# Kernel optimization log

Measured on AMD Instinct MI355X. Metric: run time of the kernel, lower is better.

The kernel has to match this reference:

```python
import jax, jax.numpy as jnp
import numpy as np

DILATIONS = (1, 2, 4, 8)
K = 3  # kernel_size
B, H, W, C = 16, 128, 128, 64
HID = 256
OUT = 64  # == C, so residual path is taken


def _depthwise(x, w, dilation):
    # x: [B,H,W,C], w: [K,K,1,C] (HWIO depthwise kernel)
    pad = dilation * (K // 2)
    return jax.lax.conv_general_dilated(
        x, w,
        window_strides=(1, 1),
        padding=[(pad, pad), (pad, pad)],
        rhs_dilation=(dilation, dilation),
        dimension_numbers=('NHWC', 'HWIO', 'NHWC'),
        feature_group_count=C,
    )


def setup_inputs() -> dict:
    key = jax.random.key(0)
    k_x, k_cw, k_w1, k_b1, k_w2, k_b2 = jax.random.split(key, 6)
    in_feat = C * (1 + len(DILATIONS))  # 320
    x = jax.random.normal(k_x, (B, H, W, C), jnp.float32)
    # depthwise kernels, one [K,K,1,C] per dilation, stacked
    conv_w = jax.random.normal(k_cw, (len(DILATIONS), K, K, 1, C), jnp.float32) * (1.0 / np.sqrt(K * K).astype(np.float32))
    W1 = jax.random.normal(k_w1, (in_feat, HID), jnp.float32) * np.float32(1.0 / np.sqrt(in_feat))
    b1 = jax.random.normal(k_b1, (HID,), jnp.float32) * 0.01
    W2 = jax.random.normal(k_w2, (HID, OUT), jnp.float32) * np.float32(1.0 / np.sqrt(HID))
    b2 = jax.random.normal(k_b2, (OUT,), jnp.float32) * 0.01
    return {"x": x, "conv_w": conv_w, "W1": W1, "b1": b1, "W2": W2, "b2": b2}


def reference(x, conv_w, W1, b1, W2, b2):
    # 1) Perception: multiscale depthwise dilated convs (same-padding per dilation)
    perceptions = [_depthwise(x, conv_w[i], d) for i, d in enumerate(DILATIONS)]
    upd_in = jnp.concatenate([x] + perceptions, axis=-1)  # [B,H,W,5C]
    # 2) Update MLP: Linear -> Dropout(eval: identity) -> GELU(exact erf) -> Linear
    h = jax.nn.gelu(upd_in @ W1 + b1, approximate=False)  # [B,H,W,HID]
    delta = h @ W2 + b2  # [B,H,W,OUT]
    # 3) out_channels == channels and (eval mode or fire_rate==1.0): plain residual
    return x + delta
```

## Files before the change

### kernel.cpp

```cpp
#include <hip/hip_runtime.h>
#include <cstdint>

#define B_   16
#define H_   128
#define W_   128
#define C_   64
#define HID_ 256
#define XELEMS (B_ * H_ * W_ * C_)

typedef _Float16 __attribute__((ext_vector_type(2))) half2v;
typedef _Float16 __attribute__((ext_vector_type(8))) half8v;
typedef __attribute__((ext_vector_type(4))) float f32x4;
typedef unsigned short ushort_t;

#define W1S_OFF 0
#define W2S_OFF 81920
#define CWH_OFF 98304
#define XH_OFF  100608
#define WS_NEED_BYTES (2u * XH_OFF + 2u * XELEMS)

__device__ __forceinline__ int hs(int row, int col) {
  return row * 256 + (((col >> 3) ^ (row & 7)) << 3) + (col & 7);
}

__device__ __forceinline__ float fast_gelu(float h) {
  float u = h * fmaf(h * h, 0.10293921f, 2.30211813f);
  float e = exp2f(-u);
  return h * __builtin_amdgcn_rcpf(1.0f + e);
}

__global__ void cvt_x_kernel(const float* __restrict__ x,
                             _Float16* __restrict__ xh) {
  int i = (blockIdx.x * 256 + threadIdx.x) * 8;
  const float4 a = *(const float4*)&x[i];
  const float4 b = *(const float4*)&x[i + 4];
  half8v o = {(_Float16)a.x, (_Float16)a.y, (_Float16)a.z, (_Float16)a.w,
              (_Float16)b.x, (_Float16)b.y, (_Float16)b.z, (_Float16)b.w};
  *(half8v*)&xh[i] = o;
}

__global__ void cvt_weights_kernel(const float* __restrict__ W1,
                                   const float* __restrict__ W2,
                                   const float* __restrict__ cw,
                                   _Float16* __restrict__ w1s,
                                   _Float16* __restrict__ w2s,
                                   _Float16* __restrict__ cwh) {
  int t = blockIdx.x * 256 + threadIdx.x;
  if (t < 81920) {
    int j = t & 7, lane = (t >> 3) & 63, n16 = (t >> 9) & 15, ks = t >> 13;
    int k = ks * 32 + (lane >> 4) * 8 + j;
    int n = n16 * 16 + (lane & 15);
    w1s[t] = (_Float16)W1[k * 256 + n];
  } else if (t < 98304) {
    int t2 = t - 81920;
    int j = t2 & 7, lane = (t2 >> 3) & 63, n16 = (t2 >> 9) & 3, ks = t2 >> 11;
    int k = ks * 32 + (lane >> 4) * 8 + j;
    int n = n16 * 16 + (lane & 15);
    w2s[t2] = (_Float16)W2[k * 64 + n];
  } else if (t < 98304 + 2304) {
    int t3 = t - 98304;
    cwh[t3] = (_Float16)cw[t3];
  }
}

template <bool BOUND, bool FP16X>
__device__ __forceinline__ void conv_phase(const float* __restrict__ xb,
                                           const _Float16* __restrict__ xhb,
                                           const _Float16* __restrict__ cwh,
                                           ushort_t* __restrict__ feat,
                                           int tid, int tileX, int tileY) {
  const int quad = tid & 15;
  const int p0   = tid >> 4;
#pragma unroll
  for (int dd = 0; dd < 4; ++dd) {
    const int dil = 1 << dd;
    half2v w01[9], w23[9];
#pragma unroll
    for (int t = 0; t < 9; ++t) {
      uint2 wr = *(const uint2*)&cwh[(dd * 9 + t) * C_ + quad * 4];
      w01[t] = __builtin_bit_cast(half2v, wr.x);
      w23[t] = __builtin_bit_cast(half2v, wr.y);
    }
#pragma unroll
    for (int i = 0; i < 4; ++i) {
      const int p  = i * 16 + p0;
      const int py = p >> 3, px = p & 7;
      const int y0 = tileY + py, x0 = tileX + px;
      half2v a01 = {0, 0}, a23 = {0, 0};
#pragma unroll
      for (int ky = 0; ky < 3; ++ky) {
        const int yy = y0 + (ky - 1) * dil;
        if (BOUND && (unsigned)yy >= (unsigned)H_) continue;
#pragma unroll
        for (int kx = 0; kx < 3; ++kx) {
          const int xx = x0 + (kx - 1) * dil;
          if (BOUND && (unsigned)xx >= (unsigned)W_) continue;
          const int t = ky * 3 + kx;
          if (FP16X) {
            uint2 v = *(const uint2*)&xhb[(yy * W_ + xx) * C_ + quad * 4];
            a01 += __builtin_bit_cast(half2v, v.x) * w01[t];
            a23 += __builtin_bit_cast(half2v, v.y) * w23[t];
          } else {
            const float4 xv = *(const float4*)&xb[(yy * W_ + xx) * C_ + quad * 4];
            half2v xl = {(_Float16)xv.x, (_Float16)xv.y};
            half2v xh2 = {(_Float16)xv.z, (_Float16)xv.w};
            a01 += xl * w01[t];
            a23 += xh2 * w23[t];
          }
        }
      }
      uint2 pk;
      pk.x = __builtin_bit_cast(uint32_t, a01);
      pk.y = __builtin_bit_cast(uint32_t, a23);
      *(uint2*)&feat[hs(p, dd * 64 + quad * 4)] = pk;
    }
  }
}

template <bool FP16X>
__global__ __launch_bounds__(256, 4)
void nca_fused_kernel(const float* __restrict__ x,
                      const _Float16* __restrict__ xh,
                      const _Float16* __restrict__ cwh,
                      const float* __restrict__ b1,
                      const float* __restrict__ b2,
                      const _Float16* __restrict__ w1s,
                      const _Float16* __restrict__ w2s,
                      float* __restrict__ out) {
  __shared__ __align__(16) ushort_t smem[64 * 256];

  const int tid   = threadIdx.x;
  const int tileX = blockIdx.x * 8;
  const int tileY = blockIdx.y * 8;
  const int batch = blockIdx.z;
  const float*    xb  = x  + (size_t)batch * (H_ * W_ * C_);
  const _Float16* xhb = xh + (size_t)batch * (H_ * W_ * C_);

  const int lane = tid & 63;
  const int wv   = tid >> 6;
  const int lr   = lane & 15;
  const int lg   = lane >> 4;
  const int n0   = wv * 64;

  half8v xf[4][2];
#pragma unroll
  for (int pi = 0; pi < 4; ++pi) {
    const int p  = pi * 16 + lr;
    const int gp = (tileY + (p >> 3)) * W_ + tileX + (p & 7);
    if (FP16X) {
#pragma unroll
      for (int ks = 0; ks < 2; ++ks)
        xf[pi][ks] = *(const half8v*)&xhb[gp * C_ + ks * 32 + lg * 8];
    } else {
#pragma unroll
      for (int ks = 0; ks < 2; ++ks) {
        const float* bp = &xb[gp * C_ + ks * 32 + lg * 8];
        float4 u = *(const float4*)bp, v = *(const float4*)(bp + 4);
        half8v s = {(_Float16)u.x, (_Float16)u.y, (_Float16)u.z, (_Float16)u.w,
                    (_Float16)v.x, (_Float16)v.y, (_Float16)v.z, (_Float16)v.w};
        xf[pi][ks] = s;
      }
    }
  }

  const bool interior = (tileX >= 8) && (tileX <= W_ - 16) &&
                        (tileY >= 8) && (tileY <= H_ - 16);
  if (interior)
    conv_phase<false, FP16X>(xb, xhb, cwh, smem, tid, tileX, tileY);
  else
    conv_phase<true, FP16X>(xb, xhb, cwh, smem, tid, tileX, tileY);
  __syncthreads();

  f32x4 acc[4][4];
#pragma unroll
  for (int hi = 0; hi < 4; ++hi)
#pragma unroll
    for (int pi = 0; pi < 4; ++pi) acc[hi][pi] = 0;

  const half8v* w1v = (const half8v*)w1s;
#pragma unroll
  for (int ks = 0; ks < 2; ++ks) {
    half8v wf[4];
#pragma unroll
    for (int hi = 0; hi < 4; ++hi)
      wf[hi] = w1v[(ks * 16 + wv * 4 + hi) * 64 + lane];
#pragma unroll
    for (int hi = 0; hi < 4; ++hi)
#pragma unroll
      for (int pi = 0; pi < 4; ++pi)
        acc[hi][pi] = __builtin_amdgcn_mfma_f32_16x16x32_f16(
            wf[hi], xf[pi][ks], acc[hi][pi], 0, 0, 0);
  }
  for (int ks = 2; ks < 10; ++ks) {
    half8v ff[4], wf[4];
#pragma unroll
    for (int pi = 0; pi < 4; ++pi)
      ff[pi] = *(const half8v*)&smem[hs(pi * 16 + lr, (ks - 2) * 32 + lg * 8)];
#pragma unroll
    for (int hi = 0; hi < 4; ++hi)
      wf[hi] = w1v[(ks * 16 + wv * 4 + hi) * 64 + lane];
#pragma unroll
    for (int hi = 0; hi < 4; ++hi)
#pragma unroll
      for (int pi = 0; pi < 4; ++pi)
        acc[hi][pi] = __builtin_amdgcn_mfma_f32_16x16x32_f16(
            wf[hi], ff[pi], acc[hi][pi], 0, 0, 0);
  }

  float4 bias1[4];
#pragma unroll
  for (int hi = 0; hi < 4; ++hi)
    bias1[hi] = *(const float4*)&b1[n0 + hi * 16 + lg * 4];

  __syncthreads();

#pragma unroll
  for (int hi = 0; hi < 4; ++hi) {
#pragma unroll
    for (int pi = 0; pi < 4; ++pi) {
      _Float16 g[4];
#pragma unroll
      for (int q = 0; q < 4; ++q)
        g[q] = (_Float16)fast_gelu(acc[hi][pi][q] + bias1[hi][q]);
      half2v g01 = {g[0], g[1]}, g23 = {g[2], g[3]};
      uint2 pk;
      pk.x = __builtin_bit_cast(uint32_t, g01);
      pk.y = __builtin_bit_cast(uint32_t, g23);
      *(uint2*)&smem[hs(pi * 16 + lr, n0 + hi * 16 + lg * 4)] = pk;
    }
  }
  __syncthreads();

  const int m0 = wv * 16;
  f32x4 acc2[4];
#pragma unroll
  for (int ni = 0; ni < 4; ++ni) acc2[ni] = 0;

  const half8v* w2v = (const half8v*)w2s;
  for (int ks = 0; ks < 8; ++ks) {
    half8v a2 = *(const half8v*)&smem[hs(m0 + lr, ks * 32 + lg * 8)];
#pragma unroll
    for (int ni = 0; ni < 4; ++ni) {
      half8v bfr = w2v[(ks * 4 + ni) * 64 + lane];
      acc2[ni] = __builtin_amdgcn_mfma_f32_16x16x32_f16(a2, bfr, acc2[ni],
                                                        0, 0, 0);
    }
  }

#pragma unroll
  for (int ni = 0; ni < 4; ++ni) {
    const int col  = ni * 16 + lr;
    const float bias = b2[col];
#pragma unroll
    for (int q = 0; q < 4; ++q) {
      const int row = m0 + lg * 4 + q;
      const int py = row >> 3, px = row & 7;
      const size_t idx =
          ((size_t)(batch * H_ + tileY + py) * W_ + (tileX + px)) * C_ + col;
      float xr = FP16X ? (float)xh[idx] : x[idx];
      out[idx] = xr + acc2[ni][q] + bias;
    }
  }
}

extern "C" void kernel_launch(void* const* d_in, const int* in_sizes, int n_in,
                              void* d_out, int out_size, void* d_ws,
                              size_t ws_size, hipStream_t stream) {
  const float* x  = (const float*)d_in[0];
  const float* cw = (const float*)d_in[1];
  const float* W1 = (const float*)d_in[2];
  const float* b1 = (const float*)d_in[3];
  const float* W2 = (const float*)d_in[4];
  const float* b2 = (const float*)d_in[5];
  float* out = (float*)d_out;

  _Float16* wsb = (_Float16*)d_ws;
  _Float16* w1s = wsb + W1S_OFF;
  _Float16* w2s = wsb + W2S_OFF;
  _Float16* cwh = wsb + CWH_OFF;
  _Float16* xh  = wsb + XH_OFF;

  cvt_weights_kernel<<<393, 256, 0, stream>>>(W1, W2, cw, w1s, w2s, cwh);

  const bool fp16x = ws_size >= (size_t)WS_NEED_BYTES;
  dim3 grid(W_ / 8, H_ / 8, B_);
  if (fp16x) {
    cvt_x_kernel<<<XELEMS / 8 / 256, 256, 0, stream>>>(x, xh);
    nca_fused_kernel<true><<<grid, 256, 0, stream>>>(x, xh, cwh, b1, b2,
                                                     w1s, w2s, out);
  } else {
    nca_fused_kernel<false><<<grid, 256, 0, stream>>>(x, xh, cwh, b1, b2,
                                                      w1s, w2s, out);
  }
}
```

Measured before the change: 220.9 us.

## Split fused conv+MLP into separate conv-feature and MLP kernels via global buffer

Replaces the single fused kernel with a conv kernel that writes fp16 perception features to a workspace buffer in an MFMA-friendly tiled layout, followed by an MLP kernel that reads them straight from global memory. The two prep kernels (weight and x conversion) are merged into one launch, and the MLP loops get unroll hints. The intent is to let the conv phase run at higher occupancy and to drop one LDS round trip and barrier. The cost is writing and reading back about 128 MB of features through global memory, plus an extra launch. The original fused path is kept as a fallback when the workspace is too small.

```diff
diff --git a/kernel.cpp b/kernel.cpp
--- a/kernel.cpp
+++ b/kernel.cpp
@@ -17,7 +17,9 @@
 #define W2S_OFF 81920
 #define CWH_OFF 98304
 #define XH_OFF  100608
-#define WS_NEED_BYTES (2u * XH_OFF + 2u * XELEMS)
+#define FEAT_OFF (XH_OFF + XELEMS)
+#define FEAT_HALVES (4096ull * 16384ull)
+#define WS_NEED_FULL (2ull * (FEAT_OFF + FEAT_HALVES))
 
 __device__ __forceinline__ int hs(int row, int col) {
   return row * 256 + (((col >> 3) ^ (row & 7)) << 3) + (col & 7);
@@ -29,48 +31,47 @@
   return h * __builtin_amdgcn_rcpf(1.0f + e);
 }
 
-__global__ void cvt_x_kernel(const float* __restrict__ x,
-                             _Float16* __restrict__ xh) {
-  int i = (blockIdx.x * 256 + threadIdx.x) * 8;
-  const float4 a = *(const float4*)&x[i];
-  const float4 b = *(const float4*)&x[i + 4];
-  half8v o = {(_Float16)a.x, (_Float16)a.y, (_Float16)a.z, (_Float16)a.w,
-              (_Float16)b.x, (_Float16)b.y, (_Float16)b.z, (_Float16)b.w};
-  *(half8v*)&xh[i] = o;
-}
-
-__global__ void cvt_weights_kernel(const float* __restrict__ W1,
-                                   const float* __restrict__ W2,
-                                   const float* __restrict__ cw,
-                                   _Float16* __restrict__ w1s,
-                                   _Float16* __restrict__ w2s,
-                                   _Float16* __restrict__ cwh) {
-  int t = blockIdx.x * 256 + threadIdx.x;
-  if (t < 81920) {
-    int j = t & 7, lane = (t >> 3) & 63, n16 = (t >> 9) & 15, ks = t >> 13;
-    int k = ks * 32 + (lane >> 4) * 8 + j;
-    int n = n16 * 16 + (lane & 15);
-    w1s[t] = (_Float16)W1[k * 256 + n];
-  } else if (t < 98304) {
-    int t2 = t - 81920;
-    int j = t2 & 7, lane = (t2 >> 3) & 63, n16 = (t2 >> 9) & 3, ks = t2 >> 11;
-    int k = ks * 32 + (lane >> 4) * 8 + j;
-    int n = n16 * 16 + (lane & 15);
-    w2s[t2] = (_Float16)W2[k * 64 + n];
-  } else if (t < 98304 + 2304) {
-    int t3 = t - 98304;
-    cwh[t3] = (_Float16)cw[t3];
-  }
-}
-
-template <bool BOUND, bool FP16X>
-__device__ __forceinline__ void conv_phase(const float* __restrict__ xb,
-                                           const _Float16* __restrict__ xhb,
+__global__ void prep_kernel(const float* __restrict__ x,
+                            const float* __restrict__ W1,
+                            const float* __restrict__ W2,
+                            const float* __restrict__ cw,
+                            _Float16* __restrict__ wsb) {
+  if (blockIdx.x < 393) {
+    int t = blockIdx.x * 256 + threadIdx.x;
+    if (t < 81920) {
+      int j = t & 7, lane = (t >> 3) & 63, n16 = (t >> 9) & 15, ks = t >> 13;
+      int k = ks * 32 + (lane >> 4) * 8 + j;
+      int n = n16 * 16 + (lane & 15);
+      wsb[W1S_OFF + t] = (_Float16)W1[k * 256 + n];
+    } else if (t < 98304) {
+      int t2 = t - 81920;
+      int j = t2 & 7, lane = (t2 >> 3) & 63, n16 = (t2 >> 9) & 3, ks = t2 >> 11;
+      int k = ks * 32 + (lane >> 4) * 8 + j;
+      int n = n16 * 16 + (lane & 15);
+      wsb[W2S_OFF + t2] = (_Float16)W2[k * 64 + n];
+    } else if (t < 98304 + 2304) {
+      int t3 = t - 98304;
+      wsb[CWH_OFF + t3] = (_Float16)cw[t3];
+    }
+  } else {
+    int i = ((blockIdx.x - 393) * 256 + threadIdx.x) * 8;
+    const float4 a = *(const float4*)&x[i];
+    const float4 b = *(const float4*)&x[i + 4];
+    half8v o = {(_Float16)a.x, (_Float16)a.y, (_Float16)a.z, (_Float16)a.w,
+                (_Float16)b.x, (_Float16)b.y, (_Float16)b.z, (_Float16)b.w};
+    *(half8v*)&wsb[XH_OFF + i] = o;
+  }
+}
+
+template <bool BOUND>
+__device__ __forceinline__ void conv_store(const _Float16* __restrict__ xhb,
                                            const _Float16* __restrict__ cwh,
-                                           ushort_t* __restrict__ feat,
+                                           _Float16* __restrict__ ft,
                                            int tid, int tileX, int tileY) {
   const int quad = tid & 15;
   const int p0   = tid >> 4;
+  const int ksq  = quad >> 3;
+  const int c32  = (quad & 7) * 4;
 #pragma unroll
   for (int dd = 0; dd < 4; ++dd) {
     const int dil = 1 << dd;
@@ -96,45 +97,55 @@
           const int xx = x0 + (kx - 1) * dil;
           if (BOUND && (unsigned)xx >= (unsigned)W_) continue;
           const int t = ky * 3 + kx;
-          if (FP16X) {
-            uint2 v = *(const uint2*)&xhb[(yy * W_ + xx) * C_ + quad * 4];
-            a01 += __builtin_bit_cast(half2v, v.x) * w01[t];
-            a23 += __builtin_bit_cast(half2v, v.y) * w23[t];
-          } else {
-            const float4 xv = *(const float4*)&xb[(yy * W_ + xx) * C_ + quad * 4];
-            half2v xl = {(_Float16)xv.x, (_Float16)xv.y};
-            half2v xh2 = {(_Float16)xv.z, (_Float16)xv.w};
-            a01 += xl * w01[t];
-            a23 += xh2 * w23[t];
-          }
+          uint2 v = *(const uint2*)&xhb[(yy * W_ + xx) * C_ + quad * 4];
+          a01 += __builtin_bit_cast(half2v, v.x) * w01[t];
+          a23 += __builtin_bit_cast(half2v, v.y) * w23[t];
         }
       }
       uint2 pk;
       pk.x = __builtin_bit_cast(uint32_t, a01);
       pk.y = __builtin_bit_cast(uint32_t, a23);
-      *(uint2*)&feat[hs(p, dd * 64 + quad * 4)] = pk;
-    }
-  }
-}
-
-template <bool FP16X>
-__global__ __launch_bounds__(256, 4)
-void nca_fused_kernel(const float* __restrict__ x,
-                      const _Float16* __restrict__ xh,
+      *(uint2*)&ft[(dd * 2 + ksq) * 2048 + p * 32 + c32] = pk;
+    }
+  }
+}
+
+__global__ __launch_bounds__(256, 6)
+void conv_feat_kernel(const _Float16* __restrict__ xh,
                       const _Float16* __restrict__ cwh,
-                      const float* __restrict__ b1,
-                      const float* __restrict__ b2,
-                      const _Float16* __restrict__ w1s,
-                      const _Float16* __restrict__ w2s,
-                      float* __restrict__ out) {
-  __shared__ __align__(16) ushort_t smem[64 * 256];
-
+                      _Float16* __restrict__ feat) {
   const int tid   = threadIdx.x;
   const int tileX = blockIdx.x * 8;
   const int tileY = blockIdx.y * 8;
   const int batch = blockIdx.z;
-  const float*    xb  = x  + (size_t)batch * (H_ * W_ * C_);
   const _Float16* xhb = xh + (size_t)batch * (H_ * W_ * C_);
+  _Float16* ft =
+      feat + ((size_t)((batch * 16 + blockIdx.y) * 16 + blockIdx.x)) * 16384;
+  const bool interior = (tileX >= 8) && (tileX <= W_ - 16) &&
+                        (tileY >= 8) && (tileY <= H_ - 16);
+  if (interior)
+    conv_store<false>(xhb, cwh, ft, tid, tileX, tileY);
+  else
+    conv_store<true>(xhb, cwh, ft, tid, tileX, tileY);
+}
+
+__global__ __launch_bounds__(256, 4)
+void mlp_kernel(const _Float16* __restrict__ xh,
+                const _Float16* __restrict__ feat,
+                const float* __restrict__ b1,
+                const float* __restrict__ b2,
+                const _Float16* __restrict__ w1s,
+                const _Float16* __restrict__ w2s,
+                float* __restrict__ out) {
+  __shared__ __align__(16) ushort_t smem[64 * 256];
+
+  const int tid   = threadIdx.x;
+  const int tileX = blockIdx.x * 8;
+  const int tileY = blockIdx.y * 8;
+  const int batch = blockIdx.z;
+  const _Float16* xhb = xh + (size_t)batch * (H_ * W_ * C_);
+  const _Float16* ftb =
+      feat + ((size_t)((batch * 16 + blockIdx.y) * 16 + blockIdx.x)) * 16384;
 
   const int lane = tid & 63;
   const int wv   = tid >> 6;
@@ -147,29 +158,10 @@
   for (int pi = 0; pi < 4; ++pi) {
     const int p  = pi * 16 + lr;
     const int gp = (tileY + (p >> 3)) * W_ + tileX + (p & 7);
-    if (FP16X) {
-#pragma unroll
-      for (int ks = 0; ks < 2; ++ks)
-        xf[pi][ks] = *(const half8v*)&xhb[gp * C_ + ks * 32 + lg * 8];
-    } else {
-#pragma unroll
-      for (int ks = 0; ks < 2; ++ks) {
-        const float* bp = &xb[gp * C_ + ks * 32 + lg * 8];
-        float4 u = *(const float4*)bp, v = *(const float4*)(bp + 4);
-        half8v s = {(_Float16)u.x, (_Float16)u.y, (_Float16)u.z, (_Float16)u.w,
-                    (_Float16)v.x, (_Float16)v.y, (_Float16)v.z, (_Float16)v.w};
-        xf[pi][ks] = s;
-      }
-    }
-  }
-
-  const bool interior = (tileX >= 8) && (tileX <= W_ - 16) &&
-                        (tileY >= 8) && (tileY <= H_ - 16);
-  if (interior)
-    conv_phase<false, FP16X>(xb, xhb, cwh, smem, tid, tileX, tileY);
-  else
-    conv_phase<true, FP16X>(xb, xhb, cwh, smem, tid, tileX, tileY);
-  __syncthreads();
+#pragma unroll
+    for (int ks = 0; ks < 2; ++ks)
+      xf[pi][ks] = *(const half8v*)&xhb[gp * C_ + ks * 32 + lg * 8];
+  }
 
   f32x4 acc[4][4];
 #pragma unroll
@@ -191,11 +183,12 @@
         acc[hi][pi] = __builtin_amdgcn_mfma_f32_16x16x32_f16(
             wf[hi], xf[pi][ks], acc[hi][pi], 0, 0, 0);
   }
+#pragma unroll 2
   for (int ks = 2; ks < 10; ++ks) {
     half8v ff[4], wf[4];
 #pragma unroll
     for (int pi = 0; pi < 4; ++pi)
-      ff[pi] = *(const half8v*)&smem[hs(pi * 16 + lr, (ks - 2) * 32 + lg * 8)];
+      ff[pi] = *(const half8v*)&ftb[(ks - 2) * 2048 + (pi * 16 + lr) * 32 + lg * 8];
 #pragma unroll
     for (int hi = 0; hi < 4; ++hi)
       wf[hi] = w1v[(ks * 16 + wv * 4 + hi) * 64 + lane];
@@ -211,8 +204,6 @@
 #pragma unroll
   for (int hi = 0; hi < 4; ++hi)
     bias1[hi] = *(const float4*)&b1[n0 + hi * 16 + lg * 4];
-
-  __syncthreads();
 
 #pragma unroll
   for (int hi = 0; hi < 4; ++hi) {
@@ -237,6 +228,7 @@
   for (int ni = 0; ni < 4; ++ni) acc2[ni] = 0;
 
   const half8v* w2v = (const half8v*)w2s;
+#pragma unroll 2
   for (int ks = 0; ks < 8; ++ks) {
     half8v a2 = *(const half8v*)&smem[hs(m0 + lr, ks * 32 + lg * 8)];
 #pragma unroll
@@ -257,8 +249,190 @@
       const int py = row >> 3, px = row & 7;
       const size_t idx =
           ((size_t)(batch * H_ + tileY + py) * W_ + (tileX + px)) * C_ + col;
-      float xr = FP16X ? (float)xh[idx] : x[idx];
-      out[idx] = xr + acc2[ni][q] + bias;
+      out[idx] = (float)xh[idx] + acc2[ni][q] + bias;
+    }
+  }
+}
+
+template <bool BOUND>
+__device__ __forceinline__ void conv_phase_f32(const float* __restrict__ xb,
+                                               const _Float16* __restrict__ cwh,
+                                               ushort_t* __restrict__ feat,
+                                               int tid, int tileX, int tileY) {
+  const int quad = tid & 15;
+  const int p0   = tid >> 4;
+#pragma unroll
+  for (int dd = 0; dd < 4; ++dd) {
+    const int dil = 1 << dd;
+    half2v w01[9], w23[9];
+#pragma unroll
+    for (int t = 0; t < 9; ++t) {
+      uint2 wr = *(const uint2*)&cwh[(dd * 9 + t) * C_ + quad * 4];
+      w01[t] = __builtin_bit_cast(half2v, wr.x);
+      w23[t] = __builtin_bit_cast(half2v, wr.y);
+    }
+#pragma unroll
+    for (int i = 0; i < 4; ++i) {
+      const int p  = i * 16 + p0;
+      const int py = p >> 3, px = p & 7;
+      const int y0 = tileY + py, x0 = tileX + px;
+      half2v a01 = {0, 0}, a23 = {0, 0};
+#pragma unroll
+      for (int ky = 0; ky < 3; ++ky) {
+        const int yy = y0 + (ky - 1) * dil;
+        if (BOUND && (unsigned)yy >= (unsigned)H_) continue;
+#pragma unroll
+        for (int kx = 0; kx < 3; ++kx) {
+          const int xx = x0 + (kx - 1) * dil;
+          if (BOUND && (unsigned)xx >= (unsigned)W_) continue;
+          const int t = ky * 3 + kx;
+          const float4 xv = *(const float4*)&xb[(yy * W_ + xx) * C_ + quad * 4];
+          half2v xl = {(_Float16)xv.x, (_Float16)xv.y};
+          half2v xh2 = {(_Float16)xv.z, (_Float16)xv.w};
+          a01 += xl * w01[t];
+          a23 += xh2 * w23[t];
+        }
+      }
+      uint2 pk;
+      pk.x = __builtin_bit_cast(uint32_t, a01);
+      pk.y = __builtin_bit_cast(uint32_t, a23);
+      *(uint2*)&feat[hs(p, dd * 64 + quad * 4)] = pk;
+    }
+  }
+}
+
+__global__ __launch_bounds__(256, 4)
+void nca_fused_fp32(const float* __restrict__ x,
+                    const _Float16* __restrict__ cwh,
+                    const float* __restrict__ b1,
+                    const float* __restrict__ b2,
+                    const _Float16* __restrict__ w1s,
+                    const _Float16* __restrict__ w2s,
+                    float* __restrict__ out) {
+  __shared__ __align__(16) ushort_t smem[64 * 256];
+
+  const int tid   = threadIdx.x;
+  const int tileX = blockIdx.x * 8;
+  const int tileY = blockIdx.y * 8;
+  const int batch = blockIdx.z;
+  const float* xb = x + (size_t)batch * (H_ * W_ * C_);
+
+  const int lane = tid & 63;
+  const int wv   = tid >> 6;
+  const int lr   = lane & 15;
+  const int lg   = lane >> 4;
+  const int n0   = wv * 64;
+
+  half8v xf[4][2];
+#pragma unroll
+  for (int pi = 0; pi < 4; ++pi) {
+    const int p  = pi * 16 + lr;
+    const int gp = (tileY + (p >> 3)) * W_ + tileX + (p & 7);
+#pragma unroll
+    for (int ks = 0; ks < 2; ++ks) {
+      const float* bp = &xb[gp * C_ + ks * 32 + lg * 8];
+      float4 u = *(const float4*)bp, v = *(const float4*)(bp + 4);
+      half8v s = {(_Float16)u.x, (_Float16)u.y, (_Float16)u.z, (_Float16)u.w,
+                  (_Float16)v.x, (_Float16)v.y, (_Float16)v.z, (_Float16)v.w};
+      xf[pi][ks] = s;
+    }
+  }
+
+  const bool interior = (tileX >= 8) && (tileX <= W_ - 16) &&
+                        (tileY >= 8) && (tileY <= H_ - 16);
+  if (interior)
+    conv_phase_f32<false>(xb, cwh, smem, tid, tileX, tileY);
+  else
+    conv_phase_f32<true>(xb, cwh, smem, tid, tileX, tileY);
+  __syncthreads();
+
+  f32x4 acc[4][4];
+#pragma unroll
+  for (int hi = 0; hi < 4; ++hi)
+#pragma unroll
+    for (int pi = 0; pi < 4; ++pi) acc[hi][pi] = 0;
+
+  const half8v* w1v = (const half8v*)w1s;
+#pragma unroll
+  for (int ks = 0; ks < 2; ++ks) {
+    half8v wf[4];
+#pragma unroll
+    for (int hi = 0; hi < 4; ++hi)
+      wf[hi] = w1v[(ks * 16 + wv * 4 + hi) * 64 + lane];
+#pragma unroll
+    for (int hi = 0; hi < 4; ++hi)
+#pragma unroll
+      for (int pi = 0; pi < 4; ++pi)
+        acc[hi][pi] = __builtin_amdgcn_mfma_f32_16x16x32_f16(
+            wf[hi], xf[pi][ks], acc[hi][pi], 0, 0, 0);
+  }
+  for (int ks = 2; ks < 10; ++ks) {
+    half8v ff[4], wf[4];
+#pragma unroll
+    for (int pi = 0; pi < 4; ++pi)
+      ff[pi] = *(const half8v*)&smem[hs(pi * 16 + lr, (ks - 2) * 32 + lg * 8)];
+#pragma unroll
+    for (int hi = 0; hi < 4; ++hi)
+      wf[hi] = w1v[(ks * 16 + wv * 4 + hi) * 64 + lane];
+#pragma unroll
+    for (int hi = 0; hi < 4; ++hi)
+#pragma unroll
+      for (int pi = 0; pi < 4; ++pi)
+        acc[hi][pi] = __builtin_amdgcn_mfma_f32_16x16x32_f16(
+            wf[hi], ff[pi], acc[hi][pi], 0, 0, 0);
+  }
+
+  float4 bias1[4];
+#pragma unroll
+  for (int hi = 0; hi < 4; ++hi)
+    bias1[hi] = *(const float4*)&b1[n0 + hi * 16 + lg * 4];
+
+  __syncthreads();
+
+#pragma unroll
+  for (int hi = 0; hi < 4; ++hi) {
+#pragma unroll
+    for (int pi = 0; pi < 4; ++pi) {
+      _Float16 g[4];
+#pragma unroll
+      for (int q = 0; q < 4; ++q)
+        g[q] = (_Float16)fast_gelu(acc[hi][pi][q] + bias1[hi][q]);
+      half2v g01 = {g[0], g[1]}, g23 = {g[2], g[3]};
+      uint2 pk;
+      pk.x = __builtin_bit_cast(uint32_t, g01);
+      pk.y = __builtin_bit_cast(uint32_t, g23);
+      *(uint2*)&smem[hs(pi * 16 + lr, n0 + hi * 16 + lg * 4)] = pk;
+    }
+  }
+  __syncthreads();
+
+  const int m0 = wv * 16;
+  f32x4 acc2[4];
+#pragma unroll
+  for (int ni = 0; ni < 4; ++ni) acc2[ni] = 0;
+
+  const half8v* w2v = (const half8v*)w2s;
+  for (int ks = 0; ks < 8; ++ks) {
+    half8v a2 = *(const half8v*)&smem[hs(m0 + lr, ks * 32 + lg * 8)];
+#pragma unroll
+    for (int ni = 0; ni < 4; ++ni) {
+      half8v bfr = w2v[(ks * 4 + ni) * 64 + lane];
+      acc2[ni] = __builtin_amdgcn_mfma_f32_16x16x32_f16(a2, bfr, acc2[ni],
+                                                        0, 0, 0);
+    }
+  }
+
+#pragma unroll
+  for (int ni = 0; ni < 4; ++ni) {
+    const int col  = ni * 16 + lr;
+    const float bias = b2[col];
+#pragma unroll
+    for (int q = 0; q < 4; ++q) {
+      const int row = m0 + lg * 4 + q;
+      const int py = row >> 3, px = row & 7;
+      const size_t idx =
+          ((size_t)(batch * H_ + tileY + py) * W_ + (tileX + px)) * C_ + col;
+      out[idx] = x[idx] + acc2[ni][q] + bias;
     }
   }
 }
@@ -274,22 +448,21 @@
   const float* b2 = (const float*)d_in[5];
   float* out = (float*)d_out;
 
-  _Float16* wsb = (_Float16*)d_ws;
-  _Float16* w1s = wsb + W1S_OFF;
-  _Float16* w2s = wsb + W2S_OFF;
-  _Float16* cwh = wsb + CWH_OFF;
-  _Float16* xh  = wsb + XH_OFF;
-
-  cvt_weights_kernel<<<393, 256, 0, stream>>>(W1, W2, cw, w1s, w2s, cwh);
-
-  const bool fp16x = ws_size >= (size_t)WS_NEED_BYTES;
+  _Float16* wsb  = (_Float16*)d_ws;
+  _Float16* w1s  = wsb + W1S_OFF;
+  _Float16* w2s  = wsb + W2S_OFF;
+  _Float16* cwh  = wsb + CWH_OFF;
+  _Float16* xh   = wsb + XH_OFF;
+  _Float16* feat = wsb + FEAT_OFF;
+
   dim3 grid(W_ / 8, H_ / 8, B_);
-  if (fp16x) {
-    cvt_x_kernel<<<XELEMS / 8 / 256, 256, 0, stream>>>(x, xh);
-    nca_fused_kernel<true><<<grid, 256, 0, stream>>>(x, xh, cwh, b1, b2,
-                                                     w1s, w2s, out);
+
+  if (ws_size >= (size_t)WS_NEED_FULL) {
+    prep_kernel<<<393 + XELEMS / 8 / 256, 256, 0, stream>>>(x, W1, W2, cw, wsb);
+    conv_feat_kernel<<<grid, 256, 0, stream>>>(xh, cwh, feat);
+    mlp_kernel<<<grid, 256, 0, stream>>>(xh, feat, b1, b2, w1s, w2s, out);
   } else {
-    nca_fused_kernel<false><<<grid, 256, 0, stream>>>(x, xh, cwh, b1, b2,
-                                                      w1s, w2s, out);
-  }
-}
+    prep_kernel<<<393, 256, 0, stream>>>(x, W1, W2, cw, wsb);
+    nca_fused_fp32<<<grid, 256, 0, stream>>>(x, cwh, b1, b2, w1s, w2s, out);
+  }
+}
```

New measurement: 235.6 us. 1.07x slower.
